# Optimization experiments

Measured on AMD Instinct MI355X. Metric: run time of the kernel, lower is better.

## Reference

```python
import jax, jax.numpy as jnp
import numpy as np

M, K, N = 16384, 2048, 2048

def setup_inputs() -> dict:
    key = jax.random.key(0)
    k1, k2 = jax.random.split(key)
    # int8 activations and int8 weights in [-127, 127)
    x = jax.random.randint(k1, (M, K), -127, 127, dtype=jnp.int32).astype(jnp.int8)
    weight = jax.random.randint(k2, (K, N), -127, 127, dtype=jnp.int32).astype(jnp.int8)
    bias = jnp.zeros((N,), dtype=jnp.float16)
    return {"x": x, "weight": weight, "bias": bias}

def reference(x, weight, bias):
    # then fused bias add in floating point.
    acc = jax.lax.dot_general(
        x, weight,
        dimension_numbers=(((1,), (0,)), ((), ())),
        preferred_element_type=jnp.int32,
    )  # [M, N] int32
    out = acc.astype(jnp.float32) + bias.astype(jnp.float32)
    return out
```

## Files before the change

### kernel.cpp

```cpp
#include <hip/hip_runtime.h>
#include <hip/hip_fp16.h>

#define M_DIM 16384
#define K_DIM 2048
#define N_DIM 2048

#define BM 256
#define BN 256
#define BK 128
#define NT (K_DIM / BK)

typedef int int4v  __attribute__((ext_vector_type(4)));
typedef int int16v __attribute__((ext_vector_type(16)));

__device__ __forceinline__ void gl_lds16(const void* g, void* l) {
    __builtin_amdgcn_global_load_lds(
        (const __attribute__((address_space(1))) void*)g,
        (__attribute__((address_space(3))) void*)l,
        16, 0, 0);
}

__device__ __forceinline__ int pack4(int4v v) {
    return (v[0] & 255) | ((v[1] & 255) << 8) | ((v[2] & 255) << 16) | (v[3] << 24);
}

__global__ void pack_x_kernel(const int* __restrict__ x, char* __restrict__ xp) {
    const int4v* src = (const int4v*)x;
    int* dst = (int*)xp;
    int base = blockIdx.x * 1024 + threadIdx.x;
#pragma unroll
    for (int j = 0; j < 4; ++j) {
        int i = base + j * 256;
        dst[i] = pack4(src[i]);
    }
}

__global__ void wt_pack_kernel(const int* __restrict__ w, char* __restrict__ wt) {
    __shared__ char tile[64][68];
    int b  = blockIdx.x;
    int k0 = (b & 31) * 64;
    int n0 = (b >> 5) * 64;
    int t  = threadIdx.x;
    int r  = t >> 2;
    int c  = (t & 3) * 16;

    const int* src = w + (size_t)(k0 + r) * N_DIM + n0 + c;
    int4v a = *(const int4v*)(src + 0);
    int4v bb = *(const int4v*)(src + 4);
    int4v cc = *(const int4v*)(src + 8);
    int4v dd = *(const int4v*)(src + 12);
    *(int*)&tile[r][c + 0]  = pack4(a);
    *(int*)&tile[r][c + 4]  = pack4(bb);
    *(int*)&tile[r][c + 8]  = pack4(cc);
    *(int*)&tile[r][c + 12] = pack4(dd);
    __syncthreads();

    char buf[16];
#pragma unroll
    for (int j = 0; j < 16; ++j) buf[j] = tile[c + j][r];
    *(int4v*)(wt + (size_t)(n0 + r) * K_DIM + k0 + c) = *(int4v*)buf;
}

__global__ __launch_bounds__(512, 2)
void gemm_i8_kernel(const char* __restrict__ A, const char* __restrict__ BT,
                    const __half* __restrict__ bias, float* __restrict__ C) {
    __shared__ char Asm[2][BM * BK];
    __shared__ char Bsm[2][BN * BK];

    const int bid = blockIdx.x;
    const int mt = bid & 63;
    const int nt = bid >> 6;
    const int R0 = mt * BM, C0 = nt * BN;

    const int t = threadIdx.x;
    const int lane = t & 63;
    const int w = t >> 6;
    const int wm = w >> 2;
    const int wn = w & 3;
    const int l31 = lane & 31, l7 = lane & 7, khl = lane >> 5;

    int16v acc[4][2];
#pragma unroll
    for (int i = 0; i < 4; ++i)
#pragma unroll
        for (int j = 0; j < 2; ++j) acc[i][j] = (int16v)0;

    unsigned aoffu[4], boffu[4];
    int ldst[4];
#pragma unroll
    for (int j = 0; j < 4; ++j) {
        int s = t + j * 512;
        int r = s >> 3;
        int cg = (s & 7) ^ (r & 7);
        aoffu[j] = (unsigned)(R0 + r) * K_DIM + cg * 16;
        boffu[j] = (unsigned)(C0 + r) * K_DIM + cg * 16;
        ldst[j] = s * 16;
    }

    int arows[4], brows[2];
#pragma unroll
    for (int i = 0; i < 4; ++i) arows[i] = (wm * 128 + i * 32 + l31) * 8;
#pragma unroll
    for (int j = 0; j < 2; ++j) brows[j] = (wn * 64 + j * 32 + l31) * 8;

#pragma unroll
    for (int j = 0; j < 4; ++j) gl_lds16(A + aoffu[j], &Asm[0][ldst[j]]);
#pragma unroll
    for (int j = 0; j < 4; ++j) gl_lds16(BT + boffu[j], &Bsm[0][ldst[j]]);
    asm volatile("s_waitcnt vmcnt(0)" ::: "memory");
    __builtin_amdgcn_s_barrier();

#define TILE(cur, kt)                                                           \
    {                                                                           \
        const int knext = ((kt) + 1) * BK;                                      \
        const bool pf = ((kt) + 1 < NT);                                        \
        _Pragma("unroll")                                                       \
        for (int ks = 0; ks < 4; ++ks) {                                        \
            int4v af[4], bf[2];                                                 \
            const int ch = (2 * ks + khl) ^ l7;                                 \
            _Pragma("unroll")                                                   \
            for (int i = 0; i < 4; ++i)                                         \
                af[i] = *(const int4v*)&Asm[cur][(arows[i] + ch) * 16];         \
            _Pragma("unroll")                                                   \
            for (int j = 0; j < 2; ++j)                                         \
                bf[j] = *(const int4v*)&Bsm[cur][(brows[j] + ch) * 16];         \
            if (ks == 0 && pf) {                                                \
                _Pragma("unroll")                                               \
                for (int j = 0; j < 4; ++j)                                     \
                    gl_lds16(A + aoffu[j] + knext, &Asm[(cur) ^ 1][ldst[j]]);   \
            }                                                                   \
            if (ks == 1 && pf) {                                                \
                _Pragma("unroll")                                               \
                for (int j = 0; j < 4; ++j)                                     \
                    gl_lds16(BT + boffu[j] + knext, &Bsm[(cur) ^ 1][ldst[j]]);  \
            }                                                                   \
            __builtin_amdgcn_s_barrier();                                       \
            asm volatile("s_waitcnt lgkmcnt(0)" ::: "memory");                  \
            __builtin_amdgcn_s_setprio(1);                                      \
            _Pragma("unroll")                                                   \
            for (int i = 0; i < 4; ++i) {                                       \
                _Pragma("unroll")                                               \
                for (int j = 0; j < 2; ++j)                                     \
                    acc[i][j] = __builtin_amdgcn_mfma_i32_32x32x32_i8(          \
                        af[i], bf[j], acc[i][j], 0, 0, 0);                      \
            }                                                                   \
            __builtin_amdgcn_s_setprio(0);                                      \
            if (ks == 3) asm volatile("s_waitcnt vmcnt(0)" ::: "memory");       \
            __builtin_amdgcn_s_barrier();                                       \
        }                                                                       \
    }

    for (int kt = 0; kt < NT; kt += 2) {
        TILE(0, kt)
        TILE(1, kt + 1)
    }
#undef TILE

    const int col = l31;
    const int rb = khl * 4;
#pragma unroll
    for (int j = 0; j < 2; ++j) {
        const int cn = C0 + wn * 64 + j * 32 + col;
        const float bv = __half2float(bias[cn]);
#pragma unroll
        for (int i = 0; i < 4; ++i) {
            const int rm = R0 + wm * 128 + i * 32 + rb;
#pragma unroll
            for (int reg = 0; reg < 16; ++reg) {
                const int row = rm + (reg & 3) + 8 * (reg >> 2);
                C[(size_t)row * N_DIM + cn] = (float)acc[i][j][reg] + bv;
            }
        }
    }
}

extern "C" void kernel_launch(void* const* d_in, const int* in_sizes, int n_in,
                              void* d_out, int out_size, void* d_ws, size_t ws_size,
                              hipStream_t stream) {
    const int* x = (const int*)d_in[0];
    const int* wgt = (const int*)d_in[1];
    const __half* bias = (const __half*)d_in[2];
    float* out = (float*)d_out;

    char* xp = (char*)d_ws;
    char* wt = (char*)d_ws + (size_t)M_DIM * K_DIM;

    pack_x_kernel<<<(M_DIM * (size_t)K_DIM) / 4 / 1024, 256, 0, stream>>>(x, xp);
    wt_pack_kernel<<<(K_DIM / 64) * (N_DIM / 64), 256, 0, stream>>>(wgt, wt);
    gemm_i8_kernel<<<(M_DIM / BM) * (N_DIM / BN), 512, 0, stream>>>(xp, wt, bias, out);
}
```

Baseline: 313.4 us.

## Switch GEMM to 4 waves with 128x128 warp tiles and BK=64

Restructures the int8 GEMM main loop to use 256 threads (4 waves), each computing a 128x128 sub-tile with a 4x4 MFMA accumulator grid, and halves the K tile to 64 with a 4-chunk XOR swizzle. Prefetch of the next tile is issued once at the top of each tile, and the per-k-step barriers and priority toggles are replaced by a single wait-and-barrier per tile. Block order is also changed so consecutive blocks share M rows across N tiles. This raises register pressure (256 accumulator VGPRs per lane) and lowers the number of waves per CU, trading latency hiding for fewer LDS reads per MFMA and less synchronization.

```diff
diff --git a/kernel.cpp b/kernel.cpp
--- a/kernel.cpp
+++ b/kernel.cpp
@@ -7,7 +7,7 @@
 
 #define BM 256
 #define BN 256
-#define BK 128
+#define BK 64
 #define NT (K_DIM / BK)
 
 typedef int int4v  __attribute__((ext_vector_type(4)));
@@ -61,93 +61,97 @@
     *(int4v*)(wt + (size_t)(n0 + r) * K_DIM + k0 + c) = *(int4v*)buf;
 }
 
-__global__ __launch_bounds__(512, 2)
+__global__ __launch_bounds__(256, 1)
 void gemm_i8_kernel(const char* __restrict__ A, const char* __restrict__ BT,
                     const __half* __restrict__ bias, float* __restrict__ C) {
     __shared__ char Asm[2][BM * BK];
     __shared__ char Bsm[2][BN * BK];
 
     const int bid = blockIdx.x;
-    const int mt = bid & 63;
-    const int nt = bid >> 6;
+    const int nt = bid & 7;
+    const int mt = bid >> 3;
     const int R0 = mt * BM, C0 = nt * BN;
 
     const int t = threadIdx.x;
     const int lane = t & 63;
     const int w = t >> 6;
-    const int wm = w >> 2;
-    const int wn = w & 3;
-    const int l31 = lane & 31, l7 = lane & 7, khl = lane >> 5;
+    const int wm = w >> 1;
+    const int wn = w & 1;
+    const int l31 = lane & 31, khl = lane >> 5;
 
-    int16v acc[4][2];
+    int16v acc[4][4];
 #pragma unroll
     for (int i = 0; i < 4; ++i)
 #pragma unroll
-        for (int j = 0; j < 2; ++j) acc[i][j] = (int16v)0;
+        for (int j = 0; j < 4; ++j) acc[i][j] = (int16v)0;
 
-    unsigned aoffu[4], boffu[4];
+    unsigned aoff[4], boff[4];
     int ldst[4];
 #pragma unroll
     for (int j = 0; j < 4; ++j) {
-        int s = t + j * 512;
-        int r = s >> 3;
-        int cg = (s & 7) ^ (r & 7);
-        aoffu[j] = (unsigned)(R0 + r) * K_DIM + cg * 16;
-        boffu[j] = (unsigned)(C0 + r) * K_DIM + cg * 16;
+        int s = t + j * 256;
+        int r = s >> 2;
+        int cg = (s & 3) ^ (r & 3);
+        aoff[j] = (unsigned)(R0 + r) * K_DIM + cg * 16;
+        boff[j] = (unsigned)(C0 + r) * K_DIM + cg * 16;
         ldst[j] = s * 16;
     }
 
-    int arows[4], brows[2];
+    int arow4[4], brow4[4];
 #pragma unroll
-    for (int i = 0; i < 4; ++i) arows[i] = (wm * 128 + i * 32 + l31) * 8;
+    for (int i = 0; i < 4; ++i) arow4[i] = (wm * 128 + i * 32 + l31) * 4;
 #pragma unroll
-    for (int j = 0; j < 2; ++j) brows[j] = (wn * 64 + j * 32 + l31) * 8;
+    for (int j = 0; j < 4; ++j) brow4[j] = (wn * 128 + j * 32 + l31) * 4;
+    const int sw0 = (khl)     ^ (l31 & 3);
+    const int sw1 = (2 + khl) ^ (l31 & 3);
 
 #pragma unroll
-    for (int j = 0; j < 4; ++j) gl_lds16(A + aoffu[j], &Asm[0][ldst[j]]);
+    for (int j = 0; j < 4; ++j) gl_lds16(A + aoff[j], &Asm[0][ldst[j]]);
 #pragma unroll
-    for (int j = 0; j < 4; ++j) gl_lds16(BT + boffu[j], &Bsm[0][ldst[j]]);
+    for (int j = 0; j < 4; ++j) gl_lds16(BT + boff[j], &Bsm[0][ldst[j]]);
     asm volatile("s_waitcnt vmcnt(0)" ::: "memory");
     __builtin_amdgcn_s_barrier();
 
 #define TILE(cur, kt)                                                           \
     {                                                                           \
-        const int knext = ((kt) + 1) * BK;                                      \
-        const bool pf = ((kt) + 1 < NT);                                        \
+        if ((kt) + 1 < NT) {                                                    \
+            const int knext = ((kt) + 1) * BK;                                  \
+            _Pragma("unroll")                                                   \
+            for (int j = 0; j < 4; ++j)                                         \
+                gl_lds16(A + aoff[j] + knext, &Asm[(cur) ^ 1][ldst[j]]);        \
+            _Pragma("unroll")                                                   \
+            for (int j = 0; j < 4; ++j)                                         \
+                gl_lds16(BT + boff[j] + knext, &Bsm[(cur) ^ 1][ldst[j]]);       \
+        }                                                                       \
+        int4v a0[4], b0[4], a1[4], b1[4];                                       \
         _Pragma("unroll")                                                       \
-        for (int ks = 0; ks < 4; ++ks) {                                        \
-            int4v af[4], bf[2];                                                 \
-            const int ch = (2 * ks + khl) ^ l7;                                 \
+        for (int i = 0; i < 4; ++i)                                             \
+            a0[i] = *(const int4v*)&Asm[cur][(arow4[i] + sw0) * 16];            \
+        _Pragma("unroll")                                                       \
+        for (int j = 0; j < 4; ++j)                                             \
+            b0[j] = *(const int4v*)&Bsm[cur][(brow4[j] + sw0) * 16];            \
+        _Pragma("unroll")                                                       \
+        for (int i = 0; i < 4; ++i)                                             \
+            a1[i] = *(const int4v*)&Asm[cur][(arow4[i] + sw1) * 16];            \
+        _Pragma("unroll")                                                       \
+        for (int j = 0; j < 4; ++j)                                             \
+            b1[j] = *(const int4v*)&Bsm[cur][(brow4[j] + sw1) * 16];            \
+        _Pragma("unroll")                                                       \
+        for (int i = 0; i < 4; ++i) {                                           \
             _Pragma("unroll")                                                   \
-            for (int i = 0; i < 4; ++i)                                         \
-                af[i] = *(const int4v*)&Asm[cur][(arows[i] + ch) * 16];         \
+            for (int j = 0; j < 4; ++j)                                         \
+                acc[i][j] = __builtin_amdgcn_mfma_i32_32x32x32_i8(              \
+                    a0[i], b0[j], acc[i][j], 0, 0, 0);                          \
+        }                                                                       \
+        _Pragma("unroll")                                                       \
+        for (int i = 0; i < 4; ++i) {                                           \
             _Pragma("unroll")                                                   \
-            for (int j = 0; j < 2; ++j)                                         \
-                bf[j] = *(const int4v*)&Bsm[cur][(brows[j] + ch) * 16];         \
-            if (ks == 0 && pf) {                                                \
-                _Pragma("unroll")                                               \
-                for (int j = 0; j < 4; ++j)                                     \
-                    gl_lds16(A + aoffu[j] + knext, &Asm[(cur) ^ 1][ldst[j]]);   \
-            }                                                                   \
-            if (ks == 1 && pf) {                                                \
-                _Pragma("unroll")                                               \
-                for (int j = 0; j < 4; ++j)                                     \
-                    gl_lds16(BT + boffu[j] + knext, &Bsm[(cur) ^ 1][ldst[j]]);  \
-            }                                                                   \
-            __builtin_amdgcn_s_barrier();                                       \
-            asm volatile("s_waitcnt lgkmcnt(0)" ::: "memory");                  \
-            __builtin_amdgcn_s_setprio(1);                                      \
-            _Pragma("unroll")                                                   \
-            for (int i = 0; i < 4; ++i) {                                       \
-                _Pragma("unroll")                                               \
-                for (int j = 0; j < 2; ++j)                                     \
-                    acc[i][j] = __builtin_amdgcn_mfma_i32_32x32x32_i8(          \
-                        af[i], bf[j], acc[i][j], 0, 0, 0);                      \
-            }                                                                   \
-            __builtin_amdgcn_s_setprio(0);                                      \
-            if (ks == 3) asm volatile("s_waitcnt vmcnt(0)" ::: "memory");       \
-            __builtin_amdgcn_s_barrier();                                       \
+            for (int j = 0; j < 4; ++j)                                         \
+                acc[i][j] = __builtin_amdgcn_mfma_i32_32x32x32_i8(              \
+                    a1[i], b1[j], acc[i][j], 0, 0, 0);                          \
         }                                                                       \
+        asm volatile("s_waitcnt vmcnt(0)" ::: "memory");                        \
+        __builtin_amdgcn_s_barrier();                                           \
     }
 
     for (int kt = 0; kt < NT; kt += 2) {
@@ -159,8 +163,8 @@
     const int col = l31;
     const int rb = khl * 4;
 #pragma unroll
-    for (int j = 0; j < 2; ++j) {
-        const int cn = C0 + wn * 64 + j * 32 + col;
+    for (int j = 0; j < 4; ++j) {
+        const int cn = C0 + wn * 128 + j * 32 + col;
         const float bv = __half2float(bias[cn]);
 #pragma unroll
         for (int i = 0; i < 4; ++i) {
@@ -187,5 +191,5 @@
 
     pack_x_kernel<<<(M_DIM * (size_t)K_DIM) / 4 / 1024, 256, 0, stream>>>(x, xp);
     wt_pack_kernel<<<(K_DIM / 64) * (N_DIM / 64), 256, 0, stream>>>(wgt, wt);
-    gemm_i8_kernel<<<(M_DIM / BM) * (N_DIM / BN), 512, 0, stream>>>(xp, wt, bias, out);
+    gemm_i8_kernel<<<(M_DIM / BM) * (N_DIM / BN), 256, 0, stream>>>(xp, wt, bias, out);
 }
```

New measurement: 378.7 us. 1.21x slower.
